# Kernel optimization log

Hardware: AMD Instinct MI355X
Metric: run time of the kernel (lower is better)

Reference implementation:

```python
import jax, jax.numpy as jnp
import numpy as np

N, E, IN_FEATS, HID, CLS, K = 100000, 3200000, 500, 64, 40, 10
EPS = 1e-8

def _col_normalize(x):
    # column-wise L2 norm over nodes (dim=0), clamped at 1e-8
    return x / jnp.clip(jnp.linalg.norm(x, axis=0), EPS, None)

def setup_inputs() -> dict:
    key = jax.random.key(0)
    ks = jax.random.split(key, 9)
    features = jax.random.normal(ks[0], (N, IN_FEATS), jnp.float32)
    noise = jax.random.normal(ks[1], (N, HID), jnp.float32)
    edge_index = jax.random.randint(ks[2], (2, E), 0, N, dtype=jnp.int32)
    norm_A = jax.random.uniform(ks[3], (E,), jnp.float32) * 0.1  # normalized adj weights
    W1 = jax.random.normal(ks[4], (IN_FEATS, HID), jnp.float32) * (1.0 / np.sqrt(IN_FEATS))
    b1 = jax.random.normal(ks[5], (HID,), jnp.float32) * 0.01
    W2 = jax.random.normal(ks[6], (HID, CLS), jnp.float32) * (1.0 / np.sqrt(HID))
    b2 = jax.random.normal(ks[7], (CLS,), jnp.float32) * 0.01
    alpha = jax.random.normal(ks[8], (HID, K + 1), jnp.float32) * 0.1
    return {"features": features, "noise": noise, "norm_A": norm_A, "W1": W1,
            "b1": b1, "W2": W2, "b2": b2, "alpha": alpha, "edge_index": edge_index}

def reference(features, noise, norm_A, W1, b1, W2, b2, alpha, edge_index):
    # fc1 + act (dropout p=0 -> identity)
    x = jax.nn.relu(features @ W1 + b1)
    x = x + noise * 1e-5  # blank_noise = randn_like(x) * 1e-5
    h0 = _col_normalize(x)
    rst = alpha[:, 0] * h0  # broadcast per-channel over nodes
    last_h = h0
    second_last_h = jnp.zeros_like(h0)
    src, dst = edge_index[0], edge_index[1]
    for i in range(1, K + 1):
        # NormalBasisConv: h = A @ last_h (sparse), orthogonalize vs last two, column-normalize
        h = jax.ops.segment_sum(norm_A[:, None] * last_h[src], dst, num_segments=N)  # [N, HID]
        h = h - jnp.sum(h * last_h, axis=0) * last_h
        h = h - jnp.sum(h * second_last_h, axis=0) * second_last_h
        h = _col_normalize(h)
        rst = rst + alpha[:, i] * h
        second_last_h, last_h = last_h, h
    return rst @ W2 + b2
```

## Files before the change

kernel.cpp:

```cpp
#include <hip/hip_runtime.h>
#include <stdint.h>

#define N_NODES 100000
#define N_EDGES 3200000
#define IN_FEATS 500
#define HID 64
#define CLS 40
#define KHOPS 10
#define KT 32

__global__ void zero_kernel(float4* __restrict__ p, size_t n4) {
  size_t i = (size_t)blockIdx.x * blockDim.x + threadIdx.x;
  size_t stride = (size_t)gridDim.x * blockDim.x;
  float4 z = make_float4(0.f, 0.f, 0.f, 0.f);
  for (; i < n4; i += stride) p[i] = z;
}

__global__ void hist_kernel(const int* __restrict__ dst, int* __restrict__ off) {
  int i = blockIdx.x * blockDim.x + threadIdx.x;
  int stride = gridDim.x * blockDim.x;
  for (int e = i; e < N_EDGES; e += stride) atomicAdd(&off[dst[e] + 1], 1);
}

__launch_bounds__(1024)
__global__ void scan_kernel(int* __restrict__ off, int* __restrict__ cursor) {
  __shared__ int sums[1024];
  const int M = N_NODES + 1;
  int t = threadIdx.x;
  int chunk = (M + 1023) / 1024;
  int beg = t * chunk;
  int end = beg + chunk; if (end > M) end = M;
  int s = 0;
  for (int i = beg; i < end; ++i) s += off[i];
  sums[t] = s;
  __syncthreads();
  for (int d = 1; d < 1024; d <<= 1) {
    int v = (t >= d) ? sums[t - d] : 0;
    __syncthreads();
    sums[t] += v;
    __syncthreads();
  }
  int run = (t == 0) ? 0 : sums[t - 1];
  for (int i = beg; i < end; ++i) {
    run += off[i];
    off[i] = run;
    if (i < N_NODES) cursor[i] = run;
  }
}

__global__ void fill_kernel(const int* __restrict__ src, const int* __restrict__ dst,
                            const float* __restrict__ w, int* __restrict__ cursor,
                            int2* __restrict__ edges) {
  int i = blockIdx.x * blockDim.x + threadIdx.x;
  int stride = gridDim.x * blockDim.x;
  for (int e = i; e < N_EDGES; e += stride) {
    int p = atomicAdd(&cursor[dst[e]], 1);
    edges[p] = make_int2(src[e], __float_as_int(w[e]));
  }
}

__launch_bounds__(256)
__global__ void fc1_kernel(const float* __restrict__ F, const float* __restrict__ W1,
                           const float* __restrict__ bias1, const float* __restrict__ noise,
                           float* __restrict__ x, float* __restrict__ nn0) {
  __shared__ float Fs[KT][132];
  __shared__ float Ws[KT][64];
  __shared__ float red[64];
  const int t = threadIdx.x;
  const int tx = t & 15;
  const int ty = t >> 4;
  const int c0 = tx * 4;
  const int n0 = ty * 8;
  const int nodeBase = blockIdx.x * 128;
  const int fk = (t & 7) * 4;
  const int fn = t >> 3;
  const int wr = t >> 3;
  const int wc = (t & 7) * 8;

  float4 fr[4];
  float4 w0r, w1r;

  {
    const int kb = 0;
#pragma unroll
    for (int p = 0; p < 4; ++p) {
      int n = nodeBase + fn + 32 * p;
      int k = kb + fk;
      float4 v = make_float4(0.f, 0.f, 0.f, 0.f);
      if (n < N_NODES && k + 3 < IN_FEATS) v = *(const float4*)(F + (size_t)n * IN_FEATS + k);
      fr[p] = v;
    }
    int k = kb + wr;
    float4 a = make_float4(0.f, 0.f, 0.f, 0.f), b = a;
    if (k < IN_FEATS) {
      a = *(const float4*)(W1 + (size_t)k * HID + wc);
      b = *(const float4*)(W1 + (size_t)k * HID + wc + 4);
    }
    w0r = a; w1r = b;
  }

  float acc[8][4];
#pragma unroll
  for (int i = 0; i < 8; ++i)
#pragma unroll
    for (int j = 0; j < 4; ++j) acc[i][j] = 0.f;

  const int NTILE = (IN_FEATS + KT - 1) / KT;
  for (int tile = 0; tile < NTILE; ++tile) {
    __syncthreads();
#pragma unroll
    for (int p = 0; p < 4; ++p) {
      Fs[fk + 0][fn + 32 * p] = fr[p].x;
      Fs[fk + 1][fn + 32 * p] = fr[p].y;
      Fs[fk + 2][fn + 32 * p] = fr[p].z;
      Fs[fk + 3][fn + 32 * p] = fr[p].w;
    }
    *(float4*)&Ws[wr][wc] = w0r;
    *(float4*)&Ws[wr][wc + 4] = w1r;
    __syncthreads();
    if (tile + 1 < NTILE) {
      const int kb = (tile + 1) * KT;
#pragma unroll
      for (int p = 0; p < 4; ++p) {
        int n = nodeBase + fn + 32 * p;
        int k = kb + fk;
        float4 v = make_float4(0.f, 0.f, 0.f, 0.f);
        if (n < N_NODES && k + 3 < IN_FEATS) v = *(const float4*)(F + (size_t)n * IN_FEATS + k);
        fr[p] = v;
      }
      int k = kb + wr;
      float4 a = make_float4(0.f, 0.f, 0.f, 0.f), b = a;
      if (k < IN_FEATS) {
        a = *(const float4*)(W1 + (size_t)k * HID + wc);
        b = *(const float4*)(W1 + (size_t)k * HID + wc + 4);
      }
      w0r = a; w1r = b;
    }
#pragma unroll 8
    for (int kk = 0; kk < KT; ++kk) {
      float4 fa = *(float4*)&Fs[kk][n0];
      float4 fb = *(float4*)&Fs[kk][n0 + 4];
      float4 wv = *(float4*)&Ws[kk][c0];
      acc[0][0] = fmaf(fa.x, wv.x, acc[0][0]); acc[0][1] = fmaf(fa.x, wv.y, acc[0][1]);
      acc[0][2] = fmaf(fa.x, wv.z, acc[0][2]); acc[0][3] = fmaf(fa.x, wv.w, acc[0][3]);
      acc[1][0] = fmaf(fa.y, wv.x, acc[1][0]); acc[1][1] = fmaf(fa.y, wv.y, acc[1][1]);
      acc[1][2] = fmaf(fa.y, wv.z, acc[1][2]); acc[1][3] = fmaf(fa.y, wv.w, acc[1][3]);
      acc[2][0] = fmaf(fa.z, wv.x, acc[2][0]); acc[2][1] = fmaf(fa.z, wv.y, acc[2][1]);
      acc[2][2] = fmaf(fa.z, wv.z, acc[2][2]); acc[2][3] = fmaf(fa.z, wv.w, acc[2][3]);
      acc[3][0] = fmaf(fa.w, wv.x, acc[3][0]); acc[3][1] = fmaf(fa.w, wv.y, acc[3][1]);
      acc[3][2] = fmaf(fa.w, wv.z, acc[3][2]); acc[3][3] = fmaf(fa.w, wv.w, acc[3][3]);
      acc[4][0] = fmaf(fb.x, wv.x, acc[4][0]); acc[4][1] = fmaf(fb.x, wv.y, acc[4][1]);
      acc[4][2] = fmaf(fb.x, wv.z, acc[4][2]); acc[4][3] = fmaf(fb.x, wv.w, acc[4][3]);
      acc[5][0] = fmaf(fb.y, wv.x, acc[5][0]); acc[5][1] = fmaf(fb.y, wv.y, acc[5][1]);
      acc[5][2] = fmaf(fb.y, wv.z, acc[5][2]); acc[5][3] = fmaf(fb.y, wv.w, acc[5][3]);
      acc[6][0] = fmaf(fb.z, wv.x, acc[6][0]); acc[6][1] = fmaf(fb.z, wv.y, acc[6][1]);
      acc[6][2] = fmaf(fb.z, wv.z, acc[6][2]); acc[6][3] = fmaf(fb.z, wv.w, acc[6][3]);
      acc[7][0] = fmaf(fb.w, wv.x, acc[7][0]); acc[7][1] = fmaf(fb.w, wv.y, acc[7][1]);
      acc[7][2] = fmaf(fb.w, wv.z, acc[7][2]); acc[7][3] = fmaf(fb.w, wv.w, acc[7][3]);
    }
  }

  float4 bb = *(const float4*)(bias1 + c0);
  float np0 = 0.f, np1 = 0.f, np2 = 0.f, np3 = 0.f;
#pragma unroll
  for (int i = 0; i < 8; ++i) {
    int n = nodeBase + n0 + i;
    if (n < N_NODES) {
      float4 nz = *(const float4*)(noise + (size_t)n * HID + c0);
      float v0 = fmaxf(acc[i][0] + bb.x, 0.f) + nz.x * 1e-5f;
      float v1 = fmaxf(acc[i][1] + bb.y, 0.f) + nz.y * 1e-5f;
      float v2 = fmaxf(acc[i][2] + bb.z, 0.f) + nz.z * 1e-5f;
      float v3 = fmaxf(acc[i][3] + bb.w, 0.f) + nz.w * 1e-5f;
      *(float4*)(x + (size_t)n * HID + c0) = make_float4(v0, v1, v2, v3);
      np0 = fmaf(v0, v0, np0); np1 = fmaf(v1, v1, np1);
      np2 = fmaf(v2, v2, np2); np3 = fmaf(v3, v3, np3);
    }
  }
  if (t < 64) red[t] = 0.f;
  __syncthreads();
  atomicAdd(&red[c0 + 0], np0); atomicAdd(&red[c0 + 1], np1);
  atomicAdd(&red[c0 + 2], np2); atomicAdd(&red[c0 + 3], np3);
  __syncthreads();
  if (t < 64) atomicAdd(&nn0[t], red[t]);
}

__launch_bounds__(256)
__global__ void spmm_kernel(const int2* __restrict__ edges, const int* __restrict__ off,
                            const float* __restrict__ lastr, const float* __restrict__ secondr,
                            const float* __restrict__ nn_l,
                            float* __restrict__ h, float* __restrict__ dslot) {
  __shared__ float red[128];
  int t = threadIdx.x;
  int lane = t & 63;
  int wid = t >> 6;
  if (t < 128) red[t] = 0.f;
  __syncthreads();
  float sig = 1.f / fmaxf(sqrtf(nn_l[lane]), 1e-8f);
  float d1 = 0.f, d2 = 0.f;
  int wg = blockIdx.x * 4 + wid;
  int nw = gridDim.x * 4;
  for (int n = wg; n < N_NODES; n += nw) {
    int beg = off[n], end = off[n + 1];
    float acc = 0.f;
    for (int base = beg; base < end; base += 64) {
      int cnt = end - base; if (cnt > 64) cnt = 64;
      int li = (lane < cnt) ? lane : (cnt - 1);
      int2 e = edges[base + li];
      int j = 0;
      for (; j + 8 <= cnt; j += 8) {
        int s0 = __shfl(e.x, j + 0); float w0 = __int_as_float(__shfl(e.y, j + 0));
        int s1 = __shfl(e.x, j + 1); float w1 = __int_as_float(__shfl(e.y, j + 1));
        int s2 = __shfl(e.x, j + 2); float w2 = __int_as_float(__shfl(e.y, j + 2));
        int s3 = __shfl(e.x, j + 3); float w3 = __int_as_float(__shfl(e.y, j + 3));
        int s4 = __shfl(e.x, j + 4); float w4 = __int_as_float(__shfl(e.y, j + 4));
        int s5 = __shfl(e.x, j + 5); float w5 = __int_as_float(__shfl(e.y, j + 5));
        int s6 = __shfl(e.x, j + 6); float w6 = __int_as_float(__shfl(e.y, j + 6));
        int s7 = __shfl(e.x, j + 7); float w7 = __int_as_float(__shfl(e.y, j + 7));
        float v0 = lastr[(size_t)s0 * HID + lane];
        float v1 = lastr[(size_t)s1 * HID + lane];
        float v2 = lastr[(size_t)s2 * HID + lane];
        float v3 = lastr[(size_t)s3 * HID + lane];
        float v4 = lastr[(size_t)s4 * HID + lane];
        float v5 = lastr[(size_t)s5 * HID + lane];
        float v6 = lastr[(size_t)s6 * HID + lane];
        float v7 = lastr[(size_t)s7 * HID + lane];
        acc = fmaf(w0, v0, acc); acc = fmaf(w1, v1, acc);
        acc = fmaf(w2, v2, acc); acc = fmaf(w3, v3, acc);
        acc = fmaf(w4, v4, acc); acc = fmaf(w5, v5, acc);
        acc = fmaf(w6, v6, acc); acc = fmaf(w7, v7, acc);
      }
      for (; j < cnt; ++j) {
        int s0 = __shfl(e.x, j); float w0 = __int_as_float(__shfl(e.y, j));
        acc = fmaf(w0, lastr[(size_t)s0 * HID + lane], acc);
      }
    }
    acc *= sig;
    size_t o = (size_t)n * HID + lane;
    float l = lastr[o], s = secondr[o];
    h[o] = acc;
    d1 = fmaf(acc, l, d1);
    d2 = fmaf(acc, s, d2);
  }
  atomicAdd(&red[lane], d1);
  atomicAdd(&red[64 + lane], d2);
  __syncthreads();
  if (t < 128) atomicAdd(&dslot[t], red[t]);
}

__launch_bounds__(256)
__global__ void passB_kernel(float4* __restrict__ h4, const float4* __restrict__ l4,
                             const float4* __restrict__ s4, float* __restrict__ dcur,
                             const float* __restrict__ nn_l, const float* __restrict__ nn_s,
                             const float* __restrict__ alpha, int prevcol, int accum,
                             float4* __restrict__ rst4) {
  __shared__ float red[64];
  int t = threadIdx.x;
  int q = t & 15;
  int c0 = q * 4;
  float4 NL = ((const float4*)nn_l)[q];
  float4 NS = ((const float4*)nn_s)[q];
  float4 D1 = ((const float4*)dcur)[q];
  float4 D2 = ((const float4*)(dcur + 64))[q];
  float4 sigl, sigs;
  sigl.x = 1.f / fmaxf(sqrtf(NL.x), 1e-8f); sigl.y = 1.f / fmaxf(sqrtf(NL.y), 1e-8f);
  sigl.z = 1.f / fmaxf(sqrtf(NL.z), 1e-8f); sigl.w = 1.f / fmaxf(sqrtf(NL.w), 1e-8f);
  sigs.x = 1.f / fmaxf(sqrtf(NS.x), 1e-8f); sigs.y = 1.f / fmaxf(sqrtf(NS.y), 1e-8f);
  sigs.z = 1.f / fmaxf(sqrtf(NS.z), 1e-8f); sigs.w = 1.f / fmaxf(sqrtf(NS.w), 1e-8f);
  float4 C1, C2, AL;
  C1.x = sigl.x * sigl.x * D1.x; C1.y = sigl.y * sigl.y * D1.y;
  C1.z = sigl.z * sigl.z * D1.z; C1.w = sigl.w * sigl.w * D1.w;
  C2.x = sigs.x * sigs.x * D2.x; C2.y = sigs.y * sigs.y * D2.y;
  C2.z = sigs.z * sigs.z * D2.z; C2.w = sigs.w * sigs.w * D2.w;
  AL.x = alpha[(size_t)(c0 + 0) * (KHOPS + 1) + prevcol] * sigl.x;
  AL.y = alpha[(size_t)(c0 + 1) * (KHOPS + 1) + prevcol] * sigl.y;
  AL.z = alpha[(size_t)(c0 + 2) * (KHOPS + 1) + prevcol] * sigl.z;
  AL.w = alpha[(size_t)(c0 + 3) * (KHOPS + 1) + prevcol] * sigl.w;
  float nx = 0.f, ny = 0.f, nz = 0.f, nw = 0.f;
  int row0 = blockIdx.x * 16 + (t >> 4);
  int rstride = gridDim.x * 16;
  for (int n = row0; n < N_NODES; n += rstride) {
    size_t idx = (size_t)n * 16 + q;
    float4 h = h4[idx];
    float4 l = l4[idx];
    float4 s = s4[idx];
    h.x -= C1.x * l.x + C2.x * s.x;
    h.y -= C1.y * l.y + C2.y * s.y;
    h.z -= C1.z * l.z + C2.z * s.z;
    h.w -= C1.w * l.w + C2.w * s.w;
    h4[idx] = h;
    nx = fmaf(h.x, h.x, nx); ny = fmaf(h.y, h.y, ny);
    nz = fmaf(h.z, h.z, nz); nw = fmaf(h.w, h.w, nw);
    float4 r;
    if (accum) {
      r = rst4[idx];
      r.x = fmaf(AL.x, l.x, r.x); r.y = fmaf(AL.y, l.y, r.y);
      r.z = fmaf(AL.z, l.z, r.z); r.w = fmaf(AL.w, l.w, r.w);
    } else {
      r.x = AL.x * l.x; r.y = AL.y * l.y; r.z = AL.z * l.z; r.w = AL.w * l.w;
    }
    rst4[idx] = r;
  }
  if (t < 64) red[t] = 0.f;
  __syncthreads();
  atomicAdd(&red[c0 + 0], nx); atomicAdd(&red[c0 + 1], ny);
  atomicAdd(&red[c0 + 2], nz); atomicAdd(&red[c0 + 3], nw);
  __syncthreads();
  if (t < 64) atomicAdd(&dcur[128 + t], red[t]);
}

__launch_bounds__(256)
__global__ void gemm2_kernel(const float* __restrict__ rst, const float* __restrict__ hK,
                             const float* __restrict__ nnK, const float* __restrict__ alpha,
                             const float* __restrict__ W2, const float* __restrict__ bias2,
                             float* __restrict__ out) {
  __shared__ float W2s[HID * CLS];
  __shared__ float R[64][65];
  __shared__ float coef[64];
  int t = threadIdx.x;
  if (t < 64) coef[t] = alpha[(size_t)t * (KHOPS + 1) + KHOPS] / fmaxf(sqrtf(nnK[t]), 1e-8f);
  for (int i = t; i < HID * CLS; i += 256) W2s[i] = W2[i];
  int nodeBase = blockIdx.x * 64;
  __syncthreads();
  for (int i = t; i < 64 * 16; i += 256) {
    int r = i >> 4, c4 = (i & 15) * 4;
    int n = nodeBase + r;
    if (n < N_NODES) {
      float4 rv = *(const float4*)(rst + (size_t)n * HID + c4);
      float4 hv = *(const float4*)(hK + (size_t)n * HID + c4);
      R[r][c4 + 0] = rv.x + coef[c4 + 0] * hv.x;
      R[r][c4 + 1] = rv.y + coef[c4 + 1] * hv.y;
      R[r][c4 + 2] = rv.z + coef[c4 + 2] * hv.z;
      R[r][c4 + 3] = rv.w + coef[c4 + 3] * hv.w;
    } else {
      R[r][c4 + 0] = 0.f; R[r][c4 + 1] = 0.f; R[r][c4 + 2] = 0.f; R[r][c4 + 3] = 0.f;
    }
  }
  __syncthreads();
  int node = t >> 2;
  int cls0 = (t & 3) * 10;
  float o[10];
#pragma unroll
  for (int j = 0; j < 10; ++j) o[j] = bias2[cls0 + j];
#pragma unroll 4
  for (int k = 0; k < HID; ++k) {
    float rv = R[node][k];
    const float* wrow = &W2s[k * CLS + cls0];
#pragma unroll
    for (int j = 0; j < 10; ++j) o[j] = fmaf(rv, wrow[j], o[j]);
  }
  int n = nodeBase + node;
  if (n < N_NODES) {
#pragma unroll
    for (int j = 0; j < 10; ++j) out[(size_t)n * CLS + cls0 + j] = o[j];
  }
}

extern "C" void kernel_launch(void* const* d_in, const int* in_sizes, int n_in,
                              void* d_out, int out_size, void* d_ws, size_t ws_size,
                              hipStream_t stream) {
  (void)in_sizes; (void)n_in; (void)out_size;
  const float* features  = (const float*)d_in[0];
  const float* noise     = (const float*)d_in[1];
  const float* norm_A    = (const float*)d_in[2];
  const float* W1        = (const float*)d_in[3];
  const float* b1        = (const float*)d_in[4];
  const float* W2        = (const float*)d_in[5];
  const float* b2        = (const float*)d_in[6];
  const float* alpha     = (const float*)d_in[7];
  const int*   edge_index= (const int*)d_in[8];
  float* out = (float*)d_out;

  char* ws = (char*)d_ws;
  const size_t NB = (size_t)N_NODES * HID * sizeof(float);
  const size_t CURSOR_PAD = 400128;
  float* hA    = (float*)(ws);
  float* hC    = (float*)(ws + NB);
  float* rst   = (float*)(ws + 2 * NB);
  int2*  edges = (int2*)(ws + 3 * NB);
  int*   cursor= (int*)(ws + 4 * NB);
  char*  zbase = ws + 4 * NB + CURSOR_PAD;
  float* hB    = (float*)(zbase);
  int*   off   = (int*)(zbase + NB);
  float* dots  = (float*)(zbase + NB + 400128);
  const size_t zspan = NB + 400128 + (size_t)12 * 192 * 4;
  const size_t total = 4 * NB + CURSOR_PAD + zspan;
  if (ws_size < total) return;

  zero_kernel<<<4096, 256, 0, stream>>>((float4*)zbase, zspan / 16);
  hist_kernel<<<2048, 256, 0, stream>>>(edge_index + N_EDGES, off);
  scan_kernel<<<1, 1024, 0, stream>>>(off, cursor);
  fill_kernel<<<2048, 256, 0, stream>>>(edge_index, edge_index + N_EDGES, norm_A, cursor, edges);
  fc1_kernel<<<(N_NODES + 127) / 128, 256, 0, stream>>>(features, W1, b1, noise, hA,
                                                        dots + 1 * 192 + 128);
  float* second = hB; float* last = hA; float* cur = hC;
  for (int i = 1; i <= KHOPS; ++i) {
    float* dc = dots + (size_t)(i + 1) * 192;
    float* nl = dots + (size_t)(i)     * 192 + 128;
    float* ns = dots + (size_t)(i - 1) * 192 + 128;
    spmm_kernel<<<2048, 256, 0, stream>>>(edges, off, last, second, nl, cur, dc);
    passB_kernel<<<1024, 256, 0, stream>>>((float4*)cur, (const float4*)last,
                                           (const float4*)second, dc, nl, ns,
                                           alpha, i - 1, (i > 1) ? 1 : 0, (float4*)rst);
    float* tmp = second; second = last; last = cur; cur = tmp;
  }
  gemm2_kernel<<<(N_NODES + 63) / 64, 256, 0, stream>>>(rst, last,
                                                        dots + (size_t)(KHOPS + 1) * 192 + 128,
                                                        alpha, W2, b2, out);
}
```

Baseline: 2.922 ms.

## Partition CSR fill by destination range and use scalar edge loads in SpMM

The CSR fill kernel now assigns each block a destination-node range plus an edge slice, so atomics and scattered writes for a given range stay local and hit fewer cache lines. The SpMM kernel drops the per-chunk lane load and shuffle broadcast. It instead reads edges directly as wave-uniform loads and accumulates into eight independent partial sums to raise memory-level parallelism. In exchange, every edge's dst is read eight times during fill, and the fp32 summation order changes.

```diff
diff --git a/kernel.cpp b/kernel.cpp
--- a/kernel.cpp
+++ b/kernel.cpp
@@ -8,6 +8,7 @@
 #define CLS 40
 #define KHOPS 10
 #define KT 32
+#define NRANGE 8
 
 __global__ void zero_kernel(float4* __restrict__ p, size_t n4) {
   size_t i = (size_t)blockIdx.x * blockDim.x + threadIdx.x;
@@ -51,11 +52,20 @@
 __global__ void fill_kernel(const int* __restrict__ src, const int* __restrict__ dst,
                             const float* __restrict__ w, int* __restrict__ cursor,
                             int2* __restrict__ edges) {
-  int i = blockIdx.x * blockDim.x + threadIdx.x;
-  int stride = gridDim.x * blockDim.x;
-  for (int e = i; e < N_EDGES; e += stride) {
-    int p = atomicAdd(&cursor[dst[e]], 1);
-    edges[p] = make_int2(src[e], __float_as_int(w[e]));
+  const int r = blockIdx.x & (NRANGE - 1);
+  const int slice = blockIdx.x >> 3;
+  const int nslices = gridDim.x >> 3;
+  const int lo = r * (N_NODES / NRANGE);
+  const int hi = lo + (N_NODES / NRANGE);
+  const int per = (N_EDGES + nslices - 1) / nslices;
+  const int beg = slice * per;
+  int end = beg + per; if (end > N_EDGES) end = N_EDGES;
+  for (int e = beg + threadIdx.x; e < end; e += blockDim.x) {
+    int d = dst[e];
+    if (d >= lo && d < hi) {
+      int p = atomicAdd(&cursor[d], 1);
+      edges[p] = make_int2(src[e], __float_as_int(w[e]));
+    }
   }
 }
 
@@ -79,7 +89,6 @@
 
   float4 fr[4];
   float4 w0r, w1r;
-
   {
     const int kb = 0;
 #pragma unroll
@@ -190,50 +199,38 @@
                             const float* __restrict__ nn_l,
                             float* __restrict__ h, float* __restrict__ dslot) {
   __shared__ float red[128];
-  int t = threadIdx.x;
-  int lane = t & 63;
-  int wid = t >> 6;
+  const int t = threadIdx.x;
+  const int lane = t & 63;
+  const int wid = __builtin_amdgcn_readfirstlane(t >> 6);
   if (t < 128) red[t] = 0.f;
   __syncthreads();
-  float sig = 1.f / fmaxf(sqrtf(nn_l[lane]), 1e-8f);
+  const float sig = 1.f / fmaxf(sqrtf(nn_l[lane]), 1e-8f);
   float d1 = 0.f, d2 = 0.f;
-  int wg = blockIdx.x * 4 + wid;
-  int nw = gridDim.x * 4;
-  for (int n = wg; n < N_NODES; n += nw) {
-    int beg = off[n], end = off[n + 1];
-    float acc = 0.f;
-    for (int base = beg; base < end; base += 64) {
-      int cnt = end - base; if (cnt > 64) cnt = 64;
-      int li = (lane < cnt) ? lane : (cnt - 1);
-      int2 e = edges[base + li];
-      int j = 0;
-      for (; j + 8 <= cnt; j += 8) {
-        int s0 = __shfl(e.x, j + 0); float w0 = __int_as_float(__shfl(e.y, j + 0));
-        int s1 = __shfl(e.x, j + 1); float w1 = __int_as_float(__shfl(e.y, j + 1));
-        int s2 = __shfl(e.x, j + 2); float w2 = __int_as_float(__shfl(e.y, j + 2));
-        int s3 = __shfl(e.x, j + 3); float w3 = __int_as_float(__shfl(e.y, j + 3));
-        int s4 = __shfl(e.x, j + 4); float w4 = __int_as_float(__shfl(e.y, j + 4));
-        int s5 = __shfl(e.x, j + 5); float w5 = __int_as_float(__shfl(e.y, j + 5));
-        int s6 = __shfl(e.x, j + 6); float w6 = __int_as_float(__shfl(e.y, j + 6));
-        int s7 = __shfl(e.x, j + 7); float w7 = __int_as_float(__shfl(e.y, j + 7));
-        float v0 = lastr[(size_t)s0 * HID + lane];
-        float v1 = lastr[(size_t)s1 * HID + lane];
-        float v2 = lastr[(size_t)s2 * HID + lane];
-        float v3 = lastr[(size_t)s3 * HID + lane];
-        float v4 = lastr[(size_t)s4 * HID + lane];
-        float v5 = lastr[(size_t)s5 * HID + lane];
-        float v6 = lastr[(size_t)s6 * HID + lane];
-        float v7 = lastr[(size_t)s7 * HID + lane];
-        acc = fmaf(w0, v0, acc); acc = fmaf(w1, v1, acc);
-        acc = fmaf(w2, v2, acc); acc = fmaf(w3, v3, acc);
-        acc = fmaf(w4, v4, acc); acc = fmaf(w5, v5, acc);
-        acc = fmaf(w6, v6, acc); acc = fmaf(w7, v7, acc);
-      }
-      for (; j < cnt; ++j) {
-        int s0 = __shfl(e.x, j); float w0 = __int_as_float(__shfl(e.y, j));
-        acc = fmaf(w0, lastr[(size_t)s0 * HID + lane], acc);
-      }
-    }
+  const int nw = gridDim.x * 4;
+  for (int n = blockIdx.x * 4 + wid; n < N_NODES; n += nw) {
+    const int beg = off[n], end = off[n + 1];
+    float a0 = 0.f, a1 = 0.f, a2 = 0.f, a3 = 0.f;
+    float a4 = 0.f, a5 = 0.f, a6 = 0.f, a7 = 0.f;
+    int j = beg;
+    for (; j + 8 <= end; j += 8) {
+      int2 e0 = edges[j + 0]; int2 e1 = edges[j + 1];
+      int2 e2 = edges[j + 2]; int2 e3 = edges[j + 3];
+      int2 e4 = edges[j + 4]; int2 e5 = edges[j + 5];
+      int2 e6 = edges[j + 6]; int2 e7 = edges[j + 7];
+      a0 = fmaf(__int_as_float(e0.y), lastr[(size_t)e0.x * HID + lane], a0);
+      a1 = fmaf(__int_as_float(e1.y), lastr[(size_t)e1.x * HID + lane], a1);
+      a2 = fmaf(__int_as_float(e2.y), lastr[(size_t)e2.x * HID + lane], a2);
+      a3 = fmaf(__int_as_float(e3.y), lastr[(size_t)e3.x * HID + lane], a3);
+      a4 = fmaf(__int_as_float(e4.y), lastr[(size_t)e4.x * HID + lane], a4);
+      a5 = fmaf(__int_as_float(e5.y), lastr[(size_t)e5.x * HID + lane], a5);
+      a6 = fmaf(__int_as_float(e6.y), lastr[(size_t)e6.x * HID + lane], a6);
+      a7 = fmaf(__int_as_float(e7.y), lastr[(size_t)e7.x * HID + lane], a7);
+    }
+    for (; j < end; ++j) {
+      int2 e = edges[j];
+      a0 = fmaf(__int_as_float(e.y), lastr[(size_t)e.x * HID + lane], a0);
+    }
+    float acc = ((a0 + a1) + (a2 + a3)) + ((a4 + a5) + (a6 + a7));
     acc *= sig;
     size_t o = (size_t)n * HID + lane;
     float l = lastr[o], s = secondr[o];
```

After: 2.822 ms. -3.4%, faster.
